# Kernel tuning notes

Hardware: AMD Instinct MI355X
Metric: run time of the kernel (lower is better)

## Reference

```python
import jax, jax.numpy as jnp
import numpy as np

NC = 16       # class_nums
C = 128       # in_channel == EMBEND_DIM
NS = 8192     # support points
NQ = 30000    # query points
EPS = 1e-8


def setup_inputs() -> dict:
    key = jax.random.key(0)
    ks = jax.random.split(key, 7)
    support_features = jax.random.normal(ks[0], (NS, C), dtype=jnp.float32)
    support_labels = jax.random.randint(ks[1], (NS,), 0, NC)
    query_features = jax.random.normal(ks[2], (NQ, C), dtype=jnp.float32)
    # proj = Linear(2C+1 -> C) + ReLU + Linear(C -> 128)
    s1 = 1.0 / np.sqrt(2 * C + 1)
    W1 = jax.random.uniform(ks[3], (2 * C + 1, C), minval=-s1, maxval=s1, dtype=jnp.float32)
    b1 = jax.random.uniform(ks[4], (C,), minval=-s1, maxval=s1, dtype=jnp.float32)
    s2 = 1.0 / np.sqrt(C)
    W2 = jax.random.uniform(ks[5], (C, C), minval=-s2, maxval=s2, dtype=jnp.float32)
    b2 = jax.random.uniform(ks[6], (C,), minval=-s2, maxval=s2, dtype=jnp.float32)
    return {"support_features": support_features, "support_labels": support_labels,
            "query_features": query_features, "W1": W1, "b1": b1, "W2": W2, "b2": b2}


def _prototypes(support_features, support_labels):
    # fused scatter-mean replacing the per-class Python loop
    sums = jax.ops.segment_sum(support_features, support_labels, num_segments=NC)  # [Nc, C]
    counts = jax.ops.segment_sum(jnp.ones((support_features.shape[0],), support_features.dtype),
                                 support_labels, num_segments=NC)                   # [Nc]
    return jnp.where(counts[:, None] > 0, sums / jnp.maximum(counts, 1.0)[:, None], 0.0)


def reference(support_features, support_labels, query_features, W1, b1, W2, b2):
    protos = _prototypes(support_features, support_labels)                # [Nc, C]
    # MD_distance: cosine similarity between each query and each class prototype
    qn = query_features / jnp.maximum(jnp.linalg.norm(query_features, axis=-1, keepdims=True), EPS)
    pn = protos / jnp.maximum(jnp.linalg.norm(protos, axis=-1, keepdims=True), EPS)
    cos = jnp.einsum('qc,nc->qn', qn, pn)                                 # [Nq, Nc]
    # proj(cat([query, proto, cos], -1)) without materializing the [Nq,Nc,2C+1] concat:
    # split W1 rows into query part, proto part, and cos part.
    Wq, Wp, Wc = W1[:C], W1[C:2 * C], W1[2 * C]                           # [C,C],[C,C],[C]
    h = jax.nn.relu(jnp.einsum('qc,ch->qh', query_features, Wq)[:, None, :]
                    + jnp.einsum('nc,ch->nh', protos, Wp)[None, :, :]
                    + cos[:, :, None] * Wc[None, None, :]
                    + b1)                                                 # [Nq, Nc, C]
    similarity = jnp.einsum('qnh,ho->qno', h, W2) + b2                    # [Nq, Nc, 128]
    return similarity, cos[:, :, None]
```

## Files before the change

### kernel.cpp

```cpp
#include <hip/hip_runtime.h>

#define NQ_ 30000
#define NC_ 16
#define C_  128
#define NS_ 8192
#define QB2 32
#define NBLK2 ((NQ_ + QB2 - 1)/QB2)

typedef __attribute__((ext_vector_type(4))) float  f32x4;
typedef __attribute__((ext_vector_type(8))) short  s16x8;

#define WS_PART  0
#define WS_PCNT  65536
#define WS_T     66048
#define WS_PACK  68096

__device__ inline short f2bf(float x){
  unsigned u = __float_as_uint(x);
  u += 0x7fffu + ((u >> 16) & 1u);
  return (short)(u >> 16);
}

__global__ __launch_bounds__(256) void protoA(const float* __restrict__ sf,
                                              const int* __restrict__ lbl,
                                              const float* __restrict__ W1,
                                              const float* __restrict__ W2,
                                              float* __restrict__ ws){
  const int b = blockIdx.x;
  const int t = threadIdx.x;
  if (b < 256){
    __shared__ int ll[512];
    const int cls = b >> 4;
    const int ch  = b & 15;
    const int r0  = ch * 512;
    *(int2*)&ll[t*2] = *(const int2*)&lbl[r0 + t*2];
    __syncthreads();
    const int sub = t >> 7;
    const int c   = t & 127;
    const int i0  = sub * 256;
    float s0 = 0.f, s1 = 0.f; int cnt = 0;
    #pragma unroll 4
    for (int i = 0; i < 256; i += 2){
      if (ll[i0+i]   == cls){ s0 += sf[(size_t)(r0+i0+i  )*C_ + c]; ++cnt; }
      if (ll[i0+i+1] == cls){ s1 += sf[(size_t)(r0+i0+i+1)*C_ + c]; ++cnt; }
    }
    ws[WS_PART + ((size_t)(cls*32 + ch*2 + sub))*C_ + c] = s0 + s1;
    if (c == 0) ws[WS_PCNT + cls*32 + ch*2 + sub] = (float)cnt;
  } else {
    short* packo = (short*)(ws + WS_PACK);
    const int g0 = (b - 256)*2048 + t*8;
    const int gg = g0 & 16383;
    const int ln = (gg >> 3) & 63, ks = (gg >> 9) & 3, wvv = gg >> 11;
    const int kb = ks*32 + ((ln >> 4) & 3)*8;
    const int col = wvv*16 + (ln & 15);
    const float* src = (g0 < 16384) ? W2 : W1;
    s16x8 v;
    #pragma unroll
    for (int i = 0; i < 8; ++i) v[i] = f2bf(src[(size_t)(kb + i)*C_ + col]);
    *(s16x8*)&packo[g0] = v;
  }
}

__global__ __launch_bounds__(512) void protoB(const float* __restrict__ W1,
                                              const float* __restrict__ b1,
                                              float* __restrict__ ws){
  __shared__ float pr[C_];
  __shared__ float sacc[4][C_];
  __shared__ float rns;
  const int n = blockIdx.x;
  const int t = threadIdx.x;
  const int h = t & 127;
  const int part = t >> 7;
  if (t < 128){
    float s = 0.f, cnt = 0.f;
    #pragma unroll 8
    for (int ch = 0; ch < 32; ++ch) s   += ws[WS_PART + ((size_t)(n*32 + ch))*C_ + h];
    #pragma unroll 8
    for (int ch = 0; ch < 32; ++ch) cnt += ws[WS_PCNT + n*32 + ch];
    pr[h] = (cnt > 0.f) ? s / fmaxf(cnt, 1.f) : 0.f;
  }
  __syncthreads();
  if (t < 64){
    float q = pr[t]*pr[t] + pr[t+64]*pr[t+64];
    q += __shfl_xor(q, 1);  q += __shfl_xor(q, 2);  q += __shfl_xor(q, 4);
    q += __shfl_xor(q, 8);  q += __shfl_xor(q, 16); q += __shfl_xor(q, 32);
    if (t == 0) rns = 1.f / fmaxf(sqrtf(q), 1e-8f);
  }
  {
    float a = 0.f;
    const int c0 = part * 32;
    #pragma unroll 8
    for (int c = c0; c < c0 + 32; ++c) a = fmaf(pr[c], W1[(size_t)(C_ + c)*C_ + h], a);
    sacc[part][h] = a;
  }
  __syncthreads();
  if (t < 128){
    short* packo = (short*)(ws + WS_PACK);
    const int gg = ((h >> 5)*64 + ((h >> 3) & 3)*16 + n)*8 + (h & 7);
    packo[32768 + gg] = f2bf(pr[h] * rns);
    ws[WS_T + n*C_ + h] = b1[h] + ((sacc[0][h] + sacc[1][h]) + (sacc[2][h] + sacc[3][h]));
  }
}

__global__ __launch_bounds__(256, 3) void fused_main(const float* __restrict__ qfeat,
                                                     const float* __restrict__ W1,
                                                     const float* __restrict__ b2,
                                                     const float* __restrict__ ws,
                                                     float* __restrict__ out){
  __shared__ __align__(16) char un[16896];
  __shared__ float qw[QB2][132];
  __shared__ float tl16[NC_][132];
  __shared__ float cosl[QB2][NC_];
  __shared__ float rqn[QB2];
  __shared__ float wcl[C_];

  float (*qfs)[132] = (float(*)[132])un;
  short* hfrag = (short*)un;

  const int t    = threadIdx.x;
  const int lane = t & 63;
  const int wv   = t >> 6;
  const int fr   = lane & 15;
  const int fg   = lane >> 4;
  const int qbase = blockIdx.x * QB2;
  float* out_cos = out + (size_t)NQ_ * NC_ * C_;
  const short* pack = (const short*)(ws + WS_PACK);

  {
    const int q = t >> 3, c = (t & 7) * 16;
    int gr = qbase + q; if (gr > NQ_ - 1) gr = NQ_ - 1;
    const float* src = qfeat + (size_t)gr*C_ + c;
    *(f32x4*)&qfs[q][c]    = *(const f32x4*)(src);
    *(f32x4*)&qfs[q][c+4]  = *(const f32x4*)(src + 4);
    *(f32x4*)&qfs[q][c+8]  = *(const f32x4*)(src + 8);
    *(f32x4*)&qfs[q][c+12] = *(const f32x4*)(src + 12);
    const int r2 = t >> 4, c2 = (t & 15) * 8;
    *(f32x4*)&tl16[r2][c2]   = *(const f32x4*)(ws + WS_T + r2*C_ + c2);
    *(f32x4*)&tl16[r2][c2+4] = *(const f32x4*)(ws + WS_T + r2*C_ + c2 + 4);
    if (t < 32) *(f32x4*)&wcl[t*4] = *(const f32x4*)(W1 + 2*C_*C_ + t*4);
  }
  __syncthreads();

  {
    const int q = t >> 3, c0 = (t & 7) * 16;
    float s = 0.f;
    #pragma unroll
    for (int m = 0; m < 16; ++m){ float v = qfs[q][c0+m]; s = fmaf(v, v, s); }
    s += __shfl_xor(s, 1); s += __shfl_xor(s, 2); s += __shfl_xor(s, 4);
    if ((t & 7) == 0) rqn[q] = 1.f / fmaxf(sqrtf(s), 1e-8f);
  }

  s16x8 qfrA[4], qfrB[4];
  #pragma unroll
  for (int ks = 0; ks < 4; ++ks){
    const int c0 = ks*32 + fg*8;
    f32x4 a = *(const f32x4*)&qfs[fr][c0];
    f32x4 b = *(const f32x4*)&qfs[fr][c0+4];
    s16x8 v;
    v[0]=f2bf(a[0]); v[1]=f2bf(a[1]); v[2]=f2bf(a[2]); v[3]=f2bf(a[3]);
    v[4]=f2bf(b[0]); v[5]=f2bf(b[1]); v[6]=f2bf(b[2]); v[7]=f2bf(b[3]);
    qfrA[ks] = v;
    f32x4 a2 = *(const f32x4*)&qfs[fr+16][c0];
    f32x4 b2x = *(const f32x4*)&qfs[fr+16][c0+4];
    s16x8 w;
    w[0]=f2bf(a2[0]); w[1]=f2bf(a2[1]); w[2]=f2bf(a2[2]); w[3]=f2bf(a2[3]);
    w[4]=f2bf(b2x[0]); w[5]=f2bf(b2x[1]); w[6]=f2bf(b2x[2]); w[7]=f2bf(b2x[3]);
    qfrB[ks] = w;
  }
  s16x8 w2f[2][4];
  float b2v[2];
  #pragma unroll
  for (int j = 0; j < 2; ++j){
    const int tt = wv*2 + j;
    #pragma unroll
    for (int ks = 0; ks < 4; ++ks)
      w2f[j][ks] = *(const s16x8*)&pack[((tt*4 + ks)*64 + lane)*8];
    b2v[j] = b2[tt*16 + fr];
  }
  __syncthreads();

  #pragma unroll
  for (int g = 0; g < 2; ++g){
    #pragma unroll
    for (int j = 0; j < 2; ++j){
      const int tt = wv*2 + j;
      f32x4 dq = {0.f,0.f,0.f,0.f};
      #pragma unroll
      for (int ks = 0; ks < 4; ++ks)
        dq = __builtin_amdgcn_mfma_f32_16x16x32_bf16(g ? qfrB[ks] : qfrA[ks],
               *(const s16x8*)&pack[16384 + ((tt*4 + ks)*64 + lane)*8], dq, 0,0,0);
      #pragma unroll
      for (int r = 0; r < 4; ++r) qw[g*16 + fg*4 + r][tt*16 + fr] = dq[r];
    }
  }
  if (wv < 2){
    f32x4 dc = {0.f,0.f,0.f,0.f};
    #pragma unroll
    for (int ks = 0; ks < 4; ++ks)
      dc = __builtin_amdgcn_mfma_f32_16x16x32_bf16(wv ? qfrB[ks] : qfrA[ks],
             *(const s16x8*)&pack[32768 + (ks*64 + lane)*8], dc, 0,0,0);
    #pragma unroll
    for (int r = 0; r < 4; ++r){
      const int q = wv*16 + fg*4 + r;
      const float cv = dc[r] * rqn[q];
      cosl[q][fr] = cv;
      if (qbase + q < NQ_)
        out_cos[(size_t)(qbase + q)*NC_ + fr] = cv;
    }
  }
  __syncthreads();

  const int k0 = wv*32 + fg*8;
  const f32x4 t8a = *(const f32x4*)&tl16[fr][k0];
  const f32x4 t8b = *(const f32x4*)&tl16[fr][k0+4];
  const f32x4 w8a = *(const f32x4*)&wcl[k0];
  const f32x4 w8b = *(const f32x4*)&wcl[k0+4];

  #pragma unroll
  for (int chunk = 0; chunk < 8; ++chunk){
    const int q0 = chunk * 4;
    if (qbase + q0 >= NQ_) break;
    #pragma unroll
    for (int qq = 0; qq < 4; ++qq){
      const int q = q0 + qq;
      f32x4 qa = *(const f32x4*)&qw[q][k0];
      f32x4 qb = *(const f32x4*)&qw[q][k0+4];
      const float cv = cosl[q][fr];
      s16x8 hv;
      #pragma unroll
      for (int jj = 0; jj < 4; ++jj)
        hv[jj] = f2bf(fmaxf(fmaf(cv, w8a[jj], qa[jj] + t8a[jj]), 0.f));
      #pragma unroll
      for (int jj = 0; jj < 4; ++jj)
        hv[4+jj] = f2bf(fmaxf(fmaf(cv, w8b[jj], qb[jj] + t8b[jj]), 0.f));
      *(s16x8*)&hfrag[qq*2048 + wv*512 + lane*8] = hv;
    }
    __syncthreads();
    #pragma unroll
    for (int qq = 0; qq < 4; ++qq){
      const short* hb = &hfrag[qq*2048 + lane*8];
      s16x8 a0 = *(const s16x8*)&hb[0];
      s16x8 a1 = *(const s16x8*)&hb[512];
      s16x8 a2 = *(const s16x8*)&hb[1024];
      s16x8 a3 = *(const s16x8*)&hb[1536];
      const size_t qout = (size_t)(qbase + q0 + qq) * (NC_*C_);
      #pragma unroll
      for (int j = 0; j < 2; ++j){
        f32x4 acc = {b2v[j], b2v[j], b2v[j], b2v[j]};
        acc = __builtin_amdgcn_mfma_f32_16x16x32_bf16(a0, w2f[j][0], acc, 0,0,0);
        acc = __builtin_amdgcn_mfma_f32_16x16x32_bf16(a1, w2f[j][1], acc, 0,0,0);
        acc = __builtin_amdgcn_mfma_f32_16x16x32_bf16(a2, w2f[j][2], acc, 0,0,0);
        acc = __builtin_amdgcn_mfma_f32_16x16x32_bf16(a3, w2f[j][3], acc, 0,0,0);
        const int ocol = (wv*2 + j)*16 + fr;
        #pragma unroll
        for (int r = 0; r < 4; ++r)
          out[qout + (fg*4 + r)*C_ + ocol] = acc[r];
      }
    }
    __syncthreads();
  }
}

extern "C" void kernel_launch(void* const* d_in, const int* in_sizes, int n_in,
                              void* d_out, int out_size, void* d_ws, size_t ws_size,
                              hipStream_t stream){
  const float* sf  = (const float*)d_in[0];
  const int*   lbl = (const int*)  d_in[1];
  const float* qf  = (const float*)d_in[2];
  const float* W1  = (const float*)d_in[3];
  const float* b1  = (const float*)d_in[4];
  const float* W2  = (const float*)d_in[5];
  const float* b2  = (const float*)d_in[6];
  float* ws  = (float*)d_ws;
  float* out = (float*)d_out;

  protoA<<<272, 256, 0, stream>>>(sf, lbl, W1, W2, ws);
  protoB<<<NC_, 512, 0, stream>>>(W1, b1, ws);
  fused_main<<<NBLK2, 256, 0, stream>>>(qf, W1, b2, ws, out);
}
```

Before: 75.08 us.

## Double-buffer hidden-activation LDS tile to overlap ReLU build with MFMA

Splits the per-block query loop into 2-query chunks held in a double-buffered LDS fragment. Each iteration builds the next chunk's bf16 hidden activations while the current chunk's W2 MFMAs and output stores run, which cuts the barriers per query from two to one. The cost is twice as many loop iterations and barriers overall, with smaller chunks giving less instruction-level parallelism per step.

```diff
diff --git a/kernel.cpp b/kernel.cpp
--- a/kernel.cpp
+++ b/kernel.cpp
@@ -216,13 +216,11 @@
   const f32x4 w8a = *(const f32x4*)&wcl[k0];
   const f32x4 w8b = *(const f32x4*)&wcl[k0+4];
 
-  #pragma unroll
-  for (int chunk = 0; chunk < 8; ++chunk){
-    const int q0 = chunk * 4;
-    if (qbase + q0 >= NQ_) break;
-    #pragma unroll
-    for (int qq = 0; qq < 4; ++qq){
-      const int q = q0 + qq;
+  auto do_A = [&](int c){
+    short* hb = hfrag + (c & 1) * 4096;
+    #pragma unroll
+    for (int qq = 0; qq < 2; ++qq){
+      const int q = c*2 + qq;
       f32x4 qa = *(const f32x4*)&qw[q][k0];
       f32x4 qb = *(const f32x4*)&qw[q][k0+4];
       const float cv = cosl[q][fr];
@@ -233,17 +231,20 @@
       #pragma unroll
       for (int jj = 0; jj < 4; ++jj)
         hv[4+jj] = f2bf(fmaxf(fmaf(cv, w8b[jj], qb[jj] + t8b[jj]), 0.f));
-      *(s16x8*)&hfrag[qq*2048 + wv*512 + lane*8] = hv;
-    }
-    __syncthreads();
-    #pragma unroll
-    for (int qq = 0; qq < 4; ++qq){
-      const short* hb = &hfrag[qq*2048 + lane*8];
-      s16x8 a0 = *(const s16x8*)&hb[0];
-      s16x8 a1 = *(const s16x8*)&hb[512];
-      s16x8 a2 = *(const s16x8*)&hb[1024];
-      s16x8 a3 = *(const s16x8*)&hb[1536];
-      const size_t qout = (size_t)(qbase + q0 + qq) * (NC_*C_);
+      *(s16x8*)&hb[qq*2048 + wv*512 + lane*8] = hv;
+    }
+  };
+
+  auto do_B = [&](int c){
+    const short* hb = hfrag + (c & 1) * 4096;
+    #pragma unroll
+    for (int qq = 0; qq < 2; ++qq){
+      const short* hq = &hb[qq*2048 + lane*8];
+      s16x8 a0 = *(const s16x8*)&hq[0];
+      s16x8 a1 = *(const s16x8*)&hq[512];
+      s16x8 a2 = *(const s16x8*)&hq[1024];
+      s16x8 a3 = *(const s16x8*)&hq[1536];
+      const size_t qout = (size_t)(qbase + c*2 + qq) * (NC_*C_);
       #pragma unroll
       for (int j = 0; j < 2; ++j){
         f32x4 acc = {b2v[j], b2v[j], b2v[j], b2v[j]};
@@ -257,6 +258,16 @@
           out[qout + (fg*4 + r)*C_ + ocol] = acc[r];
       }
     }
+  };
+
+  do_A(0);
+  __syncthreads();
+  #pragma unroll 2
+  for (int c = 0; c < 16; ++c){
+    if (qbase + c*2 >= NQ_) break;
+    do_B(c);
+    if (c < 15 && qbase + (c+1)*2 < NQ_)
+      do_A(c + 1);
     __syncthreads();
   }
 }
```

Measured after the change: 80.98 us. 7.9% more time.
